# Kernel tuning notes

Hardware: AMD Instinct MI355X
Metric: run time of the kernel (lower is better)

The kernel has to match this reference:

```python
import jax, jax.numpy as jnp
import numpy as np

B, N, QD = 2, 4096, 512
HEADS, DIM_HEAD = 8, 64
INNER = HEADS * DIM_HEAD  # 512
SCALE = DIM_HEAD ** -0.5


def setup_inputs() -> dict:
    key = jax.random.key(0)
    ks = jax.random.split(key, 6)
    s = 0.02
    return {
        "x": jax.random.normal(ks[0], (B, N, QD), dtype=jnp.float32),
        "Wq": jax.random.normal(ks[1], (QD, INNER), dtype=jnp.float32) * s,
        "Wk": jax.random.normal(ks[2], (QD, INNER), dtype=jnp.float32) * s,
        "Wv": jax.random.normal(ks[3], (QD, INNER), dtype=jnp.float32) * s,
        "Wo": jax.random.normal(ks[4], (INNER, QD), dtype=jnp.float32) * s,
        "bo": jnp.zeros((QD,), dtype=jnp.float32),
    }


def reference(x, Wq, Wk, Wv, Wo, bo):
    # self-attention: context = x; mask = None; attention_sf = False
    q = x @ Wq  # [B, N, INNER]
    k = x @ Wk
    v = x @ Wv
    # split heads: [B, H, N, D]
    def split(t):
        return t.reshape(B, N, HEADS, DIM_HEAD).transpose(0, 2, 1, 3)
    q, k, v = split(q), split(k), split(v)
    # fp32 QK^T (ATTN_PRECISION='fp32' path)
    sim = jnp.einsum('bhid,bhjd->bhij', q.astype(jnp.float32), k.astype(jnp.float32)) * SCALE
    attn = jax.nn.softmax(sim, axis=-1)
    out = jnp.einsum('bhij,bhjd->bhid', attn, v)  # [B, H, N, D]
    out = out.transpose(0, 2, 1, 3).reshape(B, N, INNER)
    return out @ Wo + bo  # Dropout(p=0) is identity
```

## Files before the change

### kernel.cpp

```cpp
#include <hip/hip_runtime.h>
#include <hip/hip_bf16.h>


typedef __attribute__((ext_vector_type(8))) short short8;
typedef __attribute__((ext_vector_type(4))) float floatx4;
typedef __attribute__((ext_vector_type(16))) float floatx16;

#define MFMA16(a, b, c) __builtin_amdgcn_mfma_f32_16x16x32_bf16((a), (b), (c), 0, 0, 0)
#define MFMA32(a, b, c) __builtin_amdgcn_mfma_f32_32x32x16_bf16((a), (b), (c), 0, 0, 0)

#if __has_builtin(__builtin_amdgcn_exp2f)
#define EXP2(x) __builtin_amdgcn_exp2f(x)
#else
#define EXP2(x) exp2f(x)
#endif

#define QSCALE 0.18033688011112042f

static __device__ __forceinline__ unsigned short f2b(float f) {
  unsigned int u = __float_as_uint(f);
  u += 0x7FFFu + ((u >> 16) & 1u);
  return (unsigned short)(u >> 16);
}

static __device__ __forceinline__ unsigned int pkb(float a, float b) {
  float2 t{a, b};
  __hip_bfloat162 h = __float22bfloat162_rn(t);
  union { __hip_bfloat162 h2; unsigned int u; } cv;
  cv.h2 = h;
  return cv.u;
}

static __device__ __forceinline__ void dma16(const unsigned short* g,
                                             unsigned short* l) {
  __builtin_amdgcn_global_load_lds(
      (const __attribute__((address_space(1))) unsigned int*)g,
      (__attribute__((address_space(3))) unsigned int*)l, 16, 0, 0);
}

__global__ __launch_bounds__(256) void prep_kernel(
    const float* __restrict__ Wq, const float* __restrict__ Wk,
    const float* __restrict__ Wv, const float* __restrict__ Wo,
    const float* __restrict__ x, unsigned short* __restrict__ wtq,
    unsigned short* __restrict__ wtk, unsigned short* __restrict__ wtv,
    unsigned short* __restrict__ wto, unsigned short* __restrict__ xb) {
  const int z = blockIdx.z;
  const int tid = threadIdx.x;
  if (z >= 4) {
    const int bid = (z - 4) * 256 + blockIdx.y * 16 + blockIdx.x;
    const int idx = (bid * 256 + tid) * 8;
    const float4 a = *(const float4*)(x + idx);
    const float4 b = *(const float4*)(x + idx + 4);
    unsigned int u[4] = {pkb(a.x, a.y), pkb(a.z, a.w), pkb(b.x, b.y),
                         pkb(b.z, b.w)};
    *(short8*)(xb + idx) = *(short8*)u;
    return;
  }
  const float* __restrict__ W = (z == 0) ? Wq : (z == 1) ? Wk : (z == 2) ? Wv : Wo;
  unsigned short* __restrict__ T = (z == 0) ? wtq : (z == 1) ? wtk : (z == 2) ? wtv : wto;
  const int k0 = blockIdx.x * 32, c0 = blockIdx.y * 32;
  __shared__ float Ts[32][33];
  const int r = tid >> 3, cc = (tid & 7) * 4;
  const float4 v = *(const float4*)(W + (k0 + r) * 512 + c0 + cc);
  Ts[r][cc] = v.x; Ts[r][cc + 1] = v.y; Ts[r][cc + 2] = v.z; Ts[r][cc + 3] = v.w;
  __syncthreads();
  const unsigned long long uu =
      (unsigned long long)pkb(Ts[cc][r], Ts[cc + 1][r]) |
      ((unsigned long long)pkb(Ts[cc + 2][r], Ts[cc + 3][r]) << 32);
  *(unsigned long long*)(T + (c0 + r) * 512 + k0 + cc) = uu;
}

__global__ __launch_bounds__(256) void qkv_fused_kernel(
    const unsigned short* __restrict__ xb, const unsigned short* __restrict__ wtq,
    const unsigned short* __restrict__ wtk,
    const unsigned short* __restrict__ wtv, unsigned short* __restrict__ qo,
    unsigned short* __restrict__ ko, unsigned short* __restrict__ vo) {
  const int m0 = blockIdx.x * 128;
  const int c0 = blockIdx.y * 32;
  __shared__ __align__(16) unsigned short As[2][128 * 64];
  __shared__ __align__(16) unsigned short Bs[2][3][32 * 64];
  const int tid = threadIdx.x;
  const int lane = tid & 63, w = tid >> 6;
  const int i = lane & 15, q = lane >> 4;
  const int sl = i & 7;
  const int dr = lane >> 3, dc = lane & 7;
  const int sch = (dc ^ dr) * 8;
  const unsigned short* ag = xb + (m0 + w * 32 + dr) * 512 + sch;
  const unsigned short* bg[3];
  bg[0] = wtq + (c0 + w * 8 + dr) * 512 + sch;
  bg[1] = wtk + (c0 + w * 8 + dr) * 512 + sch;
  bg[2] = wtv + (c0 + w * 8 + dr) * 512 + sch;

  floatx4 acc[3][2][2] = {};

#pragma unroll
  for (int p = 0; p < 4; ++p) dma16(ag + p * 8 * 512, &As[0][(w * 32 + p * 8) * 64]);
#pragma unroll
  for (int z = 0; z < 3; ++z) dma16(bg[z], &Bs[0][z][(w * 8) * 64]);
  __syncthreads();

  int buf = 0;
  for (int ks = 0; ks < 8; ++ks) {
    if (ks < 7) {
      const int k1 = (ks + 1) * 64;
#pragma unroll
      for (int p = 0; p < 4; ++p)
        dma16(ag + p * 8 * 512 + k1, &As[buf ^ 1][(w * 32 + p * 8) * 64]);
#pragma unroll
      for (int z = 0; z < 3; ++z)
        dma16(bg[z] + k1, &Bs[buf ^ 1][z][(w * 8) * 64]);
    }
#pragma unroll
    for (int kc = 0; kc < 2; ++kc) {
      short8 af[2];
#pragma unroll
      for (int t = 0; t < 2; ++t)
        af[t] = *(const short8*)&As[buf][(w * 32 + t * 16 + i) * 64 +
                                        (((kc * 4 + q) ^ sl) * 8)];
#pragma unroll
      for (int z = 0; z < 3; ++z)
#pragma unroll
        for (int g = 0; g < 2; ++g) {
          const short8 bf = *(const short8*)&Bs[buf][z][(g * 16 + i) * 64 +
                                                        (((kc * 4 + q) ^ sl) * 8)];
#pragma unroll
          for (int t = 0; t < 2; ++t)
            acc[z][t][g] = MFMA16(af[t], bf, acc[z][t][g]);
        }
    }
    __syncthreads();
    buf ^= 1;
  }
#pragma unroll
  for (int z = 0; z < 3; ++z)
#pragma unroll
    for (int t = 0; t < 2; ++t)
#pragma unroll
      for (int g = 0; g < 2; ++g) {
        const int col = c0 + g * 16 + i;
        const int h = col >> 6, d = col & 63;
        const int row0 = m0 + w * 32 + t * 16 + q * 4;
        const int b = row0 >> 12;
        const int n0 = row0 & 4095;
        if (z == 2) {
          unsigned int* dst =
              (unsigned int*)&vo[(((b * 8 + h) * 64 + d) << 12) + n0];
          dst[0] = pkb(acc[z][t][g][0], acc[z][t][g][1]);
          dst[1] = pkb(acc[z][t][g][2], acc[z][t][g][3]);
        } else {
          unsigned short* dst = (z == 0) ? qo : ko;
          const float sc = (z == 0) ? QSCALE : 1.0f;
#pragma unroll
          for (int r = 0; r < 4; ++r)
            dst[(((b * 8 + h) << 12) + (n0 + r)) * 64 + d] =
                f2b(acc[z][t][g][r] * sc);
        }
      }
}

__global__ __launch_bounds__(512, 4) void flash_kernel(
    const unsigned short* __restrict__ Q, const unsigned short* __restrict__ K,
    const unsigned short* __restrict__ Vt, unsigned short* __restrict__ O) {
  const int bh = blockIdx.x;
  const int m0 = blockIdx.y * 128;
  const int tid = threadIdx.x;
  const int lane = tid & 63, w = tid >> 6;
  const int ql = lane & 31, hi = lane >> 5;
  const int rt = w & 3;
  const int kg = w >> 2;
  const unsigned short* qp = Q + bh * (4096 * 64);
  const unsigned short* kp = K + bh * (4096 * 64);
  const unsigned short* vp = Vt + bh * (64 * 4096);

  __shared__ __align__(16) unsigned short SM[32768];

  const int drow = ((w & 3) << 3) + (lane >> 3);
  const int dchk = ((lane & 7) ^ ((lane >> 3) & 7)) * 8;
  const unsigned short* kdma = kp + (kg * 2048 + drow) * 64 + dchk;
  const unsigned short* vdma = vp + drow * 4096 + kg * 2048 + dchk;
  unsigned short* kl = SM + kg * 4096 + (w & 3) * 512;
  unsigned short* vl = SM + 16384 + kg * 4096 + (w & 3) * 512;

  short8 qf[4];
  {
    const unsigned short* qrp = qp + (m0 + rt * 32 + ql) * 64 + hi * 8;
#pragma unroll
    for (int ks = 0; ks < 4; ++ks) qf[ks] = *(const short8*)(qrp + ks * 16);
  }

  floatx16 accO[2] = {};
  float accLp = 0.f;
  const int sx = ql & 7;

  dma16(kdma, kl);
  dma16(kdma + 32 * 64, kl + 32 * 64);
  dma16(vdma, vl);
  dma16(vdma + 32 * 4096, vl + 32 * 64);
  __syncthreads();

  int buf = 0;
  for (int jt = 0; jt < 32; ++jt) {
    if (jt < 31) {
      const unsigned short* kj = kdma + (jt + 1) * 4096;
      const unsigned short* vj = vdma + (jt + 1) * 64;
      unsigned short* kd = kl + (buf ^ 1) * 8192;
      unsigned short* vd = vl + (buf ^ 1) * 8192;
      dma16(kj, kd);
      dma16(kj + 32 * 64, kd + 32 * 64);
      dma16(vj, vd);
      dma16(vj + 32 * 4096, vd + 32 * 64);
    }
    const unsigned short* Ks = SM + buf * 8192 + kg * 4096;
    const unsigned short* Vs = SM + 16384 + buf * 8192 + kg * 4096;

    short8 pa[4];
#pragma unroll
    for (int kt = 0; kt < 2; ++kt) {
      floatx16 c;
#pragma unroll
      for (int j = 0; j < 16; ++j) c[j] = 0.0f;
      __builtin_amdgcn_s_setprio(1);
#pragma unroll
      for (int ks = 0; ks < 4; ++ks) {
        const short8 kf = *(const short8*)&Ks[(kt * 32 + ql) * 64 +
                                             (((2 * ks + hi) ^ sx) * 8)];
        c = MFMA32(kf, qf[ks], c);
      }
      __builtin_amdgcn_s_setprio(0);
      float e[16];
#pragma unroll
      for (int j = 0; j < 16; ++j) e[j] = EXP2(c[j]);
      accLp += (((e[0] + e[1]) + (e[2] + e[3])) +
                ((e[4] + e[5]) + (e[6] + e[7]))) +
               (((e[8] + e[9]) + (e[10] + e[11])) +
                ((e[12] + e[13]) + (e[14] + e[15])));
#pragma unroll
      for (int s2 = 0; s2 < 2; ++s2) {
        unsigned int a0 = pkb(e[8 * s2 + 0], e[8 * s2 + 1]);
        unsigned int c1 = pkb(e[8 * s2 + 2], e[8 * s2 + 3]);
        unsigned int b0 = pkb(e[8 * s2 + 4], e[8 * s2 + 5]);
        unsigned int d1 = pkb(e[8 * s2 + 6], e[8 * s2 + 7]);
        asm("v_permlane32_swap_b32 %0, %1" : "+v"(a0), "+v"(b0));
        asm("v_permlane32_swap_b32 %0, %1" : "+v"(c1), "+v"(d1));
        union { unsigned int u[4]; short8 s; } cv;
        cv.u[0] = a0; cv.u[1] = c1; cv.u[2] = b0; cv.u[3] = d1;
        pa[kt * 2 + s2] = cv.s;
      }
    }
    __builtin_amdgcn_s_setprio(1);
#pragma unroll
    for (int dt = 0; dt < 2; ++dt)
#pragma unroll
      for (int ks2 = 0; ks2 < 4; ++ks2) {
        const short8 vf = *(const short8*)&Vs[(dt * 32 + ql) * 64 +
                                              (((2 * ks2 + hi) ^ sx) * 8)];
        accO[dt] = MFMA32(pa[ks2], vf, accO[dt]);
      }
    __builtin_amdgcn_s_setprio(0);
    __syncthreads();
    buf ^= 1;
  }

  float* MB = (float*)SM;
  if (kg == 1) {
    float* dst = MB + (rt * 64 + lane) * 40;
#pragma unroll
    for (int dt = 0; dt < 2; ++dt)
#pragma unroll
      for (int r = 0; r < 16; ++r) dst[dt * 16 + r] = accO[dt][r];
    dst[32] = accLp;
  }
  __syncthreads();
  if (kg == 1) return;
  {
    const float* src = MB + (rt * 64 + lane) * 40;
#pragma unroll
    for (int dt = 0; dt < 2; ++dt)
#pragma unroll
      for (int r = 0; r < 16; ++r) accO[dt][r] += src[dt * 16 + r];
    accLp += src[32];
  }

  const float Lfull = accLp + __shfl(accLp, lane ^ 32, 64);
  const float invL = 1.0f / Lfull;
  const int b = bh >> 3, h = bh & 7;
#pragma unroll
  for (int r = 0; r < 16; ++r) {
    const int qrow = (r & 3) + 8 * (r >> 2) + 4 * hi;
    const float iv = __shfl(invL, qrow, 64);
    const int n = m0 + rt * 32 + qrow;
#pragma unroll
    for (int dt = 0; dt < 2; ++dt) {
      const int col = h * 64 + dt * 32 + ql;
      O[((b << 12) + n) * 512 + col] = f2b(accO[dt][r] * iv);
    }
  }
}

__global__ __launch_bounds__(256) void out_proj_kernel(
    const unsigned short* __restrict__ A, const unsigned short* __restrict__ wto,
    const float* __restrict__ bo, float* __restrict__ out) {
  const int m0 = blockIdx.x * 64, c0 = blockIdx.y * 64;
  __shared__ __align__(16) unsigned short As[2][64 * 64];
  __shared__ __align__(16) unsigned short Bs[2][64 * 64];
  const int tid = threadIdx.x;
  const int lane = tid & 63, w = tid >> 6;
  const int i = lane & 15, q = lane >> 4;
  const int wy = w >> 1, wx = w & 1;
  const int sl = i & 7;
  const int dr = lane >> 3, dc = lane & 7;
  const int sch = (dc ^ dr) * 8;
  const unsigned short* ag = A + (m0 + w * 16 + dr) * 512 + sch;
  const unsigned short* bg = wto + (c0 + w * 16 + dr) * 512 + sch;

  floatx4 acc[2][2] = {};
#pragma unroll
  for (int p = 0; p < 2; ++p) {
    dma16(ag + p * 8 * 512, &As[0][(w * 16 + p * 8) * 64]);
    dma16(bg + p * 8 * 512, &Bs[0][(w * 16 + p * 8) * 64]);
  }
  __syncthreads();

  int buf = 0;
  for (int ks = 0; ks < 8; ++ks) {
    if (ks < 7) {
      const int k1 = (ks + 1) * 64;
#pragma unroll
      for (int p = 0; p < 2; ++p) {
        dma16(ag + p * 8 * 512 + k1, &As[buf ^ 1][(w * 16 + p * 8) * 64]);
        dma16(bg + p * 8 * 512 + k1, &Bs[buf ^ 1][(w * 16 + p * 8) * 64]);
      }
    }
#pragma unroll
    for (int kc = 0; kc < 2; ++kc) {
      short8 af[2], bfr[2];
#pragma unroll
      for (int t = 0; t < 2; ++t)
        af[t] = *(const short8*)&As[buf][(wy * 32 + t * 16 + i) * 64 +
                                        (((kc * 4 + q) ^ sl) * 8)];
#pragma unroll
      for (int g = 0; g < 2; ++g)
        bfr[g] = *(const short8*)&Bs[buf][(wx * 32 + g * 16 + i) * 64 +
                                          (((kc * 4 + q) ^ sl) * 8)];
#pragma unroll
      for (int t = 0; t < 2; ++t)
#pragma unroll
        for (int g = 0; g < 2; ++g) acc[t][g] = MFMA16(af[t], bfr[g], acc[t][g]);
    }
    __syncthreads();
    buf ^= 1;
  }
#pragma unroll
  for (int t = 0; t < 2; ++t)
#pragma unroll
    for (int g = 0; g < 2; ++g) {
      const int col = c0 + wx * 32 + g * 16 + i;
      const float bias = bo[col];
#pragma unroll
      for (int r = 0; r < 4; ++r) {
        const int row = m0 + wy * 32 + t * 16 + q * 4 + r;
        out[row * 512 + col] = acc[t][g][r] + bias;
      }
    }
}

extern "C" void kernel_launch(void* const* d_in, const int* in_sizes, int n_in,
                              void* d_out, int out_size, void* d_ws,
                              size_t ws_size, hipStream_t stream) {
  const float* x = (const float*)d_in[0];
  const float* Wq = (const float*)d_in[1];
  const float* Wk = (const float*)d_in[2];
  const float* Wv = (const float*)d_in[3];
  const float* Wo = (const float*)d_in[4];
  const float* bo = (const float*)d_in[5];
  float* out = (float*)d_out;

  const size_t tsz = (size_t)16 * 4096 * 64;
  unsigned short* qws = (unsigned short*)d_ws;
  unsigned short* kws = qws + tsz;
  unsigned short* vws = kws + tsz;
  unsigned short* ows = vws + tsz;
  unsigned short* wtq = ows + tsz;
  unsigned short* wtk = wtq + 512 * 512;
  unsigned short* wtv = wtk + 512 * 512;
  unsigned short* wto = wtv + 512 * 512;
  unsigned short* xb = wto + 512 * 512;

  prep_kernel<<<dim3(16, 16, 12), 256, 0, stream>>>(Wq, Wk, Wv, Wo, x, wtq,
                                                    wtk, wtv, wto, xb);
  qkv_fused_kernel<<<dim3(64, 16), 256, 0, stream>>>(xb, wtq, wtk, wtv, qws,
                                                     kws, vws);
  flash_kernel<<<dim3(16, 32), 512, 0, stream>>>(qws, kws, vws, ows);
  out_proj_kernel<<<dim3(128, 8), 256, 0, stream>>>(ows, wto, bo, out);
}
```

Before: 195.7 us.

## Stage V transpose through LDS for coalesced stores; enlarge out-proj row tile

In the QKV kernel, the transposed V tile now goes into shared memory first, so each thread can write 16 contiguous bf16 values to the transposed V buffer instead of scattered 4-byte stores. The output projection kernel moves from 64x64 to 128x64 tiles, with each wave covering 32 rows across all 64 columns. This halves the grid and raises B-fragment reuse per A load. The larger tile doubles the A-tile LDS footprint and uses more accumulators, which may cut occupancy.

New measurement: 196.4 us. Within noise of the previous version (+0.3%).

```diff
diff --git a/kernel.cpp b/kernel.cpp
--- a/kernel.cpp
+++ b/kernel.cpp
@@ -131,31 +131,52 @@
     __syncthreads();
     buf ^= 1;
   }
-#pragma unroll
-  for (int z = 0; z < 3; ++z)
+
+  const int h = c0 >> 6;
+  const int b = m0 >> 12;
+  const int n0b = m0 & 4095;
+
+#pragma unroll
+  for (int z = 0; z < 2; ++z) {
+    unsigned short* dst = (z == 0) ? qo : ko;
+    const float sc = (z == 0) ? QSCALE : 1.0f;
 #pragma unroll
     for (int t = 0; t < 2; ++t)
 #pragma unroll
       for (int g = 0; g < 2; ++g) {
         const int col = c0 + g * 16 + i;
-        const int h = col >> 6, d = col & 63;
-        const int row0 = m0 + w * 32 + t * 16 + q * 4;
-        const int b = row0 >> 12;
-        const int n0 = row0 & 4095;
-        if (z == 2) {
-          unsigned int* dst =
-              (unsigned int*)&vo[(((b * 8 + h) * 64 + d) << 12) + n0];
-          dst[0] = pkb(acc[z][t][g][0], acc[z][t][g][1]);
-          dst[1] = pkb(acc[z][t][g][2], acc[z][t][g][3]);
-        } else {
-          unsigned short* dst = (z == 0) ? qo : ko;
-          const float sc = (z == 0) ? QSCALE : 1.0f;
-#pragma unroll
-          for (int r = 0; r < 4; ++r)
-            dst[(((b * 8 + h) << 12) + (n0 + r)) * 64 + d] =
-                f2b(acc[z][t][g][r] * sc);
-        }
-      }
+        const int d = col & 63;
+        const int n0 = n0b + w * 32 + t * 16 + q * 4;
+#pragma unroll
+        for (int r = 0; r < 4; ++r)
+          dst[(((b * 8 + h) << 12) + (n0 + r)) * 64 + d] =
+              f2b(acc[z][t][g][r] * sc);
+      }
+  }
+
+  {
+    unsigned short* VT = (unsigned short*)As;
+#pragma unroll
+    for (int t = 0; t < 2; ++t)
+#pragma unroll
+      for (int g = 0; g < 2; ++g) {
+        const int dl = g * 16 + i;
+        const int nl = w * 32 + t * 16 + q * 4;
+        const unsigned long long uu =
+            (unsigned long long)pkb(acc[2][t][g][0], acc[2][t][g][1]) |
+            ((unsigned long long)pkb(acc[2][t][g][2], acc[2][t][g][3]) << 32);
+        *(unsigned long long*)&VT[dl * 136 + nl] = uu;
+      }
+    __syncthreads();
+    const int dp = tid >> 3;
+    const int nc = (tid & 7) * 16;
+    const short8 v0 = *(const short8*)&VT[dp * 136 + nc];
+    const short8 v1 = *(const short8*)&VT[dp * 136 + nc + 8];
+    unsigned short* vdst =
+        vo + (size_t)(b * 8 + h) * 262144 + ((c0 & 63) + dp) * 4096 + n0b + nc;
+    *(short8*)vdst = v0;
+    *(short8*)(vdst + 8) = v1;
+  }
 }
 
 __global__ __launch_bounds__(512, 4) void flash_kernel(
@@ -300,25 +321,25 @@
 __global__ __launch_bounds__(256) void out_proj_kernel(
     const unsigned short* __restrict__ A, const unsigned short* __restrict__ wto,
     const float* __restrict__ bo, float* __restrict__ out) {
-  const int m0 = blockIdx.x * 64, c0 = blockIdx.y * 64;
-  __shared__ __align__(16) unsigned short As[2][64 * 64];
+  const int m0 = blockIdx.x * 128, c0 = blockIdx.y * 64;
+  __shared__ __align__(16) unsigned short As[2][128 * 64];
   __shared__ __align__(16) unsigned short Bs[2][64 * 64];
   const int tid = threadIdx.x;
   const int lane = tid & 63, w = tid >> 6;
   const int i = lane & 15, q = lane >> 4;
-  const int wy = w >> 1, wx = w & 1;
   const int sl = i & 7;
   const int dr = lane >> 3, dc = lane & 7;
   const int sch = (dc ^ dr) * 8;
-  const unsigned short* ag = A + (m0 + w * 16 + dr) * 512 + sch;
+  const unsigned short* ag = A + (m0 + w * 32 + dr) * 512 + sch;
   const unsigned short* bg = wto + (c0 + w * 16 + dr) * 512 + sch;
 
-  floatx4 acc[2][2] = {};
-#pragma unroll
-  for (int p = 0; p < 2; ++p) {
-    dma16(ag + p * 8 * 512, &As[0][(w * 16 + p * 8) * 64]);
+  floatx4 acc[2][4] = {};
+#pragma unroll
+  for (int p = 0; p < 4; ++p)
+    dma16(ag + p * 8 * 512, &As[0][(w * 32 + p * 8) * 64]);
+#pragma unroll
+  for (int p = 0; p < 2; ++p)
     dma16(bg + p * 8 * 512, &Bs[0][(w * 16 + p * 8) * 64]);
-  }
   __syncthreads();
 
   int buf = 0;
@@ -326,26 +347,28 @@
     if (ks < 7) {
       const int k1 = (ks + 1) * 64;
 #pragma unroll
-      for (int p = 0; p < 2; ++p) {
-        dma16(ag + p * 8 * 512 + k1, &As[buf ^ 1][(w * 16 + p * 8) * 64]);
+      for (int p = 0; p < 4; ++p)
+        dma16(ag + p * 8 * 512 + k1, &As[buf ^ 1][(w * 32 + p * 8) * 64]);
+#pragma unroll
+      for (int p = 0; p < 2; ++p)
         dma16(bg + p * 8 * 512 + k1, &Bs[buf ^ 1][(w * 16 + p * 8) * 64]);
-      }
     }
 #pragma unroll
     for (int kc = 0; kc < 2; ++kc) {
-      short8 af[2], bfr[2];
+      short8 af[2], bfr[4];
 #pragma unroll
       for (int t = 0; t < 2; ++t)
-        af[t] = *(const short8*)&As[buf][(wy * 32 + t * 16 + i) * 64 +
+        af[t] = *(const short8*)&As[buf][(w * 32 + t * 16 + i) * 64 +
                                         (((kc * 4 + q) ^ sl) * 8)];
 #pragma unroll
-      for (int g = 0; g < 2; ++g)
-        bfr[g] = *(const short8*)&Bs[buf][(wx * 32 + g * 16 + i) * 64 +
+      for (int g = 0; g < 4; ++g)
+        bfr[g] = *(const short8*)&Bs[buf][(g * 16 + i) * 64 +
                                           (((kc * 4 + q) ^ sl) * 8)];
 #pragma unroll
       for (int t = 0; t < 2; ++t)
 #pragma unroll
-        for (int g = 0; g < 2; ++g) acc[t][g] = MFMA16(af[t], bfr[g], acc[t][g]);
+        for (int g = 0; g < 4; ++g)
+          acc[t][g] = MFMA16(af[t], bfr[g], acc[t][g]);
     }
     __syncthreads();
     buf ^= 1;
@@ -353,12 +376,12 @@
 #pragma unroll
   for (int t = 0; t < 2; ++t)
 #pragma unroll
-    for (int g = 0; g < 2; ++g) {
-      const int col = c0 + wx * 32 + g * 16 + i;
+    for (int g = 0; g < 4; ++g) {
+      const int col = c0 + g * 16 + i;
       const float bias = bo[col];
 #pragma unroll
       for (int r = 0; r < 4; ++r) {
-        const int row = m0 + wy * 32 + t * 16 + q * 4 + r;
+        const int row = m0 + w * 32 + t * 16 + q * 4 + r;
         out[row * 512 + col] = acc[t][g][r] + bias;
       }
     }
@@ -391,5 +414,5 @@
   qkv_fused_kernel<<<dim3(64, 16), 256, 0, stream>>>(xb, wtq, wtk, wtv, qws,
                                                      kws, vws);
   flash_kernel<<<dim3(16, 32), 512, 0, stream>>>(qws, kws, vws, ows);
-  out_proj_kernel<<<dim3(128, 8), 256, 0, stream>>>(ows, wto, bo, out);
-}
+  out_proj_kernel<<<dim3(64, 8), 256, 0, stream>>>(ows, wto, bo, out);
+}
```
